# Kernel tuning notes

Measured on AMD Instinct MI355X. Metric: run time of the kernel, lower is better.

## Reference

```python
import jax, jax.numpy as jnp
import numpy as np

SEQ, BATCH, IN_DIM, HID_DIM = 512, 256, 256, 256
NQ = 8
ALPHA = 0.5
MLP_HID = 128


def _linear_init(key, fan_in, fan_out):
    k1, k2 = jax.random.split(key)
    bound = 1.0 / np.sqrt(fan_in)
    W = jax.random.uniform(k1, (fan_in, fan_out), minval=-bound, maxval=bound, dtype=jnp.float32)
    b = jax.random.uniform(k2, (fan_out,), minval=-bound, maxval=bound, dtype=jnp.float32)
    return W, b


def setup_inputs() -> dict:
    key = jax.random.key(0)
    ks = jax.random.split(key, 12)
    cdim = IN_DIM + HID_DIM
    inputs = jax.random.normal(ks[0], (SEQ, BATCH, IN_DIM), dtype=jnp.float32)
    W1, b1 = _linear_init(ks[1], cdim, MLP_HID)
    W2, b2 = _linear_init(ks[2], MLP_HID, NQ * 4)
    Wf, bf = _linear_init(ks[3], cdim, 1)
    Wi, bi = _linear_init(ks[4], cdim, 1)
    Wg, bg = _linear_init(ks[5], cdim, 1)
    Wo, bo = _linear_init(ks[6], cdim, 1)
    rzf = jax.random.normal(ks[7], (NQ,), dtype=jnp.float32)
    rzi = jax.random.normal(ks[8], (NQ,), dtype=jnp.float32)
    rzg = jax.random.normal(ks[9], (NQ,), dtype=jnp.float32)
    rzo = jax.random.normal(ks[10], (NQ,), dtype=jnp.float32)
    return dict(inputs=inputs, W1=W1, b1=b1, W2=W2, b2=b2,
                Wf=Wf, bf=bf, Wi=Wi, bi=bi, Wg=Wg, bg=bg, Wo=Wo, bo=bo,
                rzf=rzf, rzi=rzi, rzg=rzg, rzo=rzo)


def _qgate(theta):
    # Analytic expectations of the RX/RZ/CNOT-chain circuit:
    # <Z_k> = prod_{j<=k} cos(theta_j); rz_params cancel in Z expectations.
    # Returns mean over wires, shape (batch, 1).
    return jnp.mean(jnp.cumprod(jnp.cos(theta), axis=-1), axis=-1, keepdims=True)


def reference(inputs, W1, b1, W2, b2, Wf, bf, Wi, bi, Wg, bg, Wo, bo, rzf, rzi, rzg, rzo):
    batch = inputs.shape[1]
    hx0 = jnp.zeros((batch, HID_DIM), dtype=inputs.dtype)
    cx0 = jnp.zeros((batch, HID_DIM), dtype=inputs.dtype)

    def step(carry, x):
        hx, cx = carry
        combined = jnp.concatenate([x, hx], axis=1)  # (B, in+hid)
        f_c = jax.nn.sigmoid(combined @ Wf + bf)
        i_c = jax.nn.sigmoid(combined @ Wi + bi)
        g_c = jnp.tanh(combined @ Wg + bg)
        o_c = jax.nn.sigmoid(combined @ Wo + bo)
        h1 = jax.nn.relu(combined @ W1 + b1)
        q = h1 @ W2 + b2  # (B, 4*NQ)
        q_f = _qgate(q[:, 0 * NQ:1 * NQ])
        q_i = _qgate(q[:, 1 * NQ:2 * NQ])
        q_g = _qgate(q[:, 2 * NQ:3 * NQ])
        q_o = _qgate(q[:, 3 * NQ:4 * NQ])
        f = (1 - ALPHA) * f_c + ALPHA * jax.nn.sigmoid(q_f)
        i = (1 - ALPHA) * i_c + ALPHA * jax.nn.sigmoid(q_i)
        g = (1 - ALPHA) * g_c + ALPHA * jnp.tanh(q_g)
        o = (1 - ALPHA) * o_c + ALPHA * jax.nn.sigmoid(q_o)
        cx_new = f * cx + i * g
        hx_new = o * jnp.tanh(cx_new)
        return (hx_new, cx_new), hx_new

    (hx, cx), outputs = jax.lax.scan(step, (hx0, cx0), inputs)
    return outputs, (hx, cx)
```

## Files before the change

### kernel.cpp

```cpp
#include <hip/hip_runtime.h>

#define SEQ 512
#define BATCH 256
#define INDIM 256
#define MLP 128
#define M_ROWS (SEQ * BATCH)
#define PRE_STRIDE 136
#define AUX_OFF ((size_t)M_ROWS * PRE_STRIDE)

#define BT_OFF (AUX_OFF + 160)

typedef __attribute__((ext_vector_type(8))) short short8v;
typedef __attribute__((ext_vector_type(4))) float f32x4;

__device__ __forceinline__ unsigned short bf16_rtne(float f) {
  unsigned u = __float_as_uint(f);
  unsigned r = u + 0x7FFFu + ((u >> 16) & 1u);
  return (unsigned short)(r >> 16);
}
__device__ __forceinline__ void cvt2(float f, unsigned short& h,
                                     unsigned short& l) {
  h = bf16_rtne(f);
  l = bf16_rtne(f - __uint_as_float((unsigned)h << 16));
}

__global__ __launch_bounds__(256) void prep_kernel(
    const float* __restrict__ W1,
    const float* __restrict__ Wf, const float* __restrict__ Wi,
    const float* __restrict__ Wg, const float* __restrict__ Wo,
    const float* __restrict__ bf, const float* __restrict__ bi,
    const float* __restrict__ bg, const float* __restrict__ bo,
    const float* __restrict__ b1, float* __restrict__ aux,
    float* __restrict__ btbase) {
  const int tid = threadIdx.x;
  if (tid < 128) {
    float s = 0.f;
    for (int k = 0; k < 256; ++k) s += W1[(size_t)(256 + k) * 128 + tid];
    aux[tid] = s;
  } else if (tid < 132) {
    const int g = tid - 128;
    const float* w = (g == 0) ? Wf : (g == 1) ? Wi : (g == 2) ? Wg : Wo;
    float s = 0.f;
    for (int k = 0; k < 256; ++k) s += w[256 + k];
    aux[128 + g] = s;
  } else if (tid < 136) {
    const int g = tid - 132;
    const float* bp = (g == 0) ? bf : (g == 1) ? bi : (g == 2) ? bg : bo;
    aux[132 + g] = bp[0];
  }

  unsigned short* bth = (unsigned short*)btbase;
  unsigned short* btl = (unsigned short*)(btbase + 18432);
  float* b144 = btbase + 36864;
  for (int tau = tid; tau < 576; tau += 256) {
    const int n = tau >> 2, q = tau & 3;
    const float* wg = (n == 129) ? Wi : (n == 130) ? Wg : (n == 131) ? Wo : Wf;
    for (int k = q * 64; k < q * 64 + 64; ++k) {
      const float v = (n < 128) ? W1[(size_t)k * 128 + n]
                                : ((n < 132) ? wg[k] : 0.f);
      unsigned short h, l;
      cvt2(v, h, l);
      bth[n * 256 + k] = h;
      btl[n * 256 + k] = l;
    }
  }
  if (tid < 144) {
    const float bv = (tid < 128) ? b1[tid]
                   : (tid == 128) ? bf[0] : (tid == 129) ? bi[0]
                   : (tid == 130) ? bg[0] : (tid == 131) ? bo[0] : 0.f;
    b144[tid] = bv;
  }
}

__global__ __attribute__((amdgpu_waves_per_eu(1, 3))) __launch_bounds__(256)
void gemm_kernel(const float* __restrict__ X,
                 const unsigned short* __restrict__ Bth,
                 const unsigned short* __restrict__ Btl,
                 const float* __restrict__ bias144,
                 float* __restrict__ PRE) {
  __shared__ __align__(16) unsigned short Ah[4096];
  __shared__ __align__(16) unsigned short Al[4096];
  __shared__ __align__(16) unsigned short Bh[4608];
  __shared__ __align__(16) unsigned short Bl[4608];

  const int tid = threadIdx.x;
  const size_t rowbase = (size_t)blockIdx.x * 128;
  const int lane = tid & 63, wv = tid >> 6;
  const int l15 = lane & 15, kgl = lane >> 4;
  const int mt0 = wv * 2, mt1 = wv * 2 + 1;

  f32x4 acc0[9], acc1[9];
#pragma unroll
  for (int nt = 0; nt < 9; ++nt) {
    acc0[nt] = (f32x4){0.f, 0.f, 0.f, 0.f};
    acc1[nt] = (f32x4){0.f, 0.f, 0.f, 0.f};
  }

  for (int kc = 0; kc < 256; kc += 32) {
    __syncthreads();
#pragma unroll
    for (int s = 0; s < 2; ++s) {
      const int tau = tid + s * 256;
      const int r = tau >> 2, kg = tau & 3;
      const float4 xa = *(const float4*)&X[(rowbase + r) * 256 + kc + kg * 8];
      const float4 xb =
          *(const float4*)&X[(rowbase + r) * 256 + kc + kg * 8 + 4];
      unsigned short h0, h1, h2, h3, h4, h5, h6, h7;
      unsigned short l0, l1, l2, l3, l4, l5, l6, l7;
      cvt2(xa.x, h0, l0); cvt2(xa.y, h1, l1);
      cvt2(xa.z, h2, l2); cvt2(xa.w, h3, l3);
      cvt2(xb.x, h4, l4); cvt2(xb.y, h5, l5);
      cvt2(xb.z, h6, l6); cvt2(xb.w, h7, l7);
      const short8v hv = {(short)h0, (short)h1, (short)h2, (short)h3,
                          (short)h4, (short)h5, (short)h6, (short)h7};
      const short8v lv = {(short)l0, (short)l1, (short)l2, (short)l3,
                          (short)l4, (short)l5, (short)l6, (short)l7};
      const int dst = (((r >> 4) * 4 + kg) * 16 + (r & 15)) * 8;
      *(short8v*)&Ah[dst] = hv;
      *(short8v*)&Al[dst] = lv;
    }
#pragma unroll
    for (int s = 0; s < 3; ++s) {
      const int tau = tid + s * 256;
      if (tau < 576) {
        const int n = tau >> 2, kg = tau & 3;
        const int src = n * 256 + kc + kg * 8;
        const int dst = (((n >> 4) * 4 + kg) * 16 + (n & 15)) * 8;
        *(short8v*)&Bh[dst] = *(const short8v*)&Bth[src];
        *(short8v*)&Bl[dst] = *(const short8v*)&Btl[src];
      }
    }
    __syncthreads();

    const int ab0 = ((mt0 * 4 + kgl) * 16 + l15) * 8;
    const int ab1 = ((mt1 * 4 + kgl) * 16 + l15) * 8;
    const short8v ah0 = *(const short8v*)&Ah[ab0];
    const short8v al0 = *(const short8v*)&Al[ab0];
    const short8v ah1 = *(const short8v*)&Ah[ab1];
    const short8v al1 = *(const short8v*)&Al[ab1];
#pragma unroll
    for (int nt = 0; nt < 9; ++nt) {
      const int bb = ((nt * 4 + kgl) * 16 + l15) * 8;
      const short8v bh = *(const short8v*)&Bh[bb];
      const short8v bl = *(const short8v*)&Bl[bb];
      acc0[nt] = __builtin_amdgcn_mfma_f32_16x16x32_bf16(ah0, bh, acc0[nt], 0, 0, 0);
      acc0[nt] = __builtin_amdgcn_mfma_f32_16x16x32_bf16(ah0, bl, acc0[nt], 0, 0, 0);
      acc0[nt] = __builtin_amdgcn_mfma_f32_16x16x32_bf16(al0, bh, acc0[nt], 0, 0, 0);
      acc1[nt] = __builtin_amdgcn_mfma_f32_16x16x32_bf16(ah1, bh, acc1[nt], 0, 0, 0);
      acc1[nt] = __builtin_amdgcn_mfma_f32_16x16x32_bf16(ah1, bl, acc1[nt], 0, 0, 0);
      acc1[nt] = __builtin_amdgcn_mfma_f32_16x16x32_bf16(al1, bh, acc1[nt], 0, 0, 0);
    }
  }

#pragma unroll
  for (int nt = 0; nt < 9; ++nt) {
    const int col = nt * 16 + l15;
    if (col < 132) {
      const float bb = bias144[col];
#pragma unroll
      for (int q = 0; q < 4; ++q) {
        PRE[(rowbase + mt0 * 16 + kgl * 4 + q) * PRE_STRIDE + col] =
            acc0[nt][q] + bb;
        PRE[(rowbase + mt1 * 16 + kgl * 4 + q) * PRE_STRIDE + col] =
            acc1[nt][q] + bb;
      }
    }
  }
}

__device__ __forceinline__ float sigmoid_f(float x) {
  return __fdividef(1.0f, 1.0f + __expf(-x));
}
__device__ __forceinline__ float tanh_f(float x) {
  const float e = __expf(-2.0f * x);
  return __fdividef(1.0f - e, 1.0f + e);
}
__device__ __forceinline__ float readlane_f(float v, int lane) {
  return __int_as_float(__builtin_amdgcn_readlane(__float_as_int(v), lane));
}

__global__ __attribute__((amdgpu_waves_per_eu(1, 1))) __launch_bounds__(64)
void rec_kernel(
    const float* __restrict__ PRE, const float* __restrict__ W2,
    const float* __restrict__ b2, const float* __restrict__ aux,
    float* __restrict__ out) {
  __shared__ __align__(16) float h1s[128];

  const int l = threadIdx.x;
  const int b = blockIdx.x;
  const int m = l & 31, half = l >> 5;
  const int g = m >> 3;
  const int g8 = g * 8;

  float w2r[64];
#pragma unroll
  for (int u = 0; u < 64; ++u) w2r[u] = W2[(size_t)(half * 64 + u) * 32 + m];
  const float b2m = b2[m];
  const float2 s1 = *(const float2*)&aux[2 * l];
  const float4 sg = *(const float4*)&aux[128];

  float h = 0.f, c = 0.f;

  const float* pr0 = PRE + (size_t)b * PRE_STRIDE;
  const size_t ts = (size_t)BATCH * PRE_STRIDE;

  float2 p0 = *(const float2*)(pr0 + 0 * ts + 2 * l);
  float4 g0 = *(const float4*)(pr0 + 0 * ts + 128);
  float2 p1 = *(const float2*)(pr0 + 1 * ts + 2 * l);
  float4 g1 = *(const float4*)(pr0 + 1 * ts + 128);

  const float4* h1p = (const float4*)&h1s[half * 64];

  for (int t = 0; t < SEQ; ++t) {
    const float h10 = fmaxf(fmaf(h, s1.x, p0.x), 0.f);
    const float h11 = fmaxf(fmaf(h, s1.y, p0.y), 0.f);

    ((float2*)h1s)[l] = make_float2(h10, h11);
    asm volatile("" ::: "memory");

    const float zf = fmaf(h, sg.x, g0.x);
    const float zi = fmaf(h, sg.y, g0.y);
    const float zg = fmaf(h, sg.z, g0.z);
    const float zo = fmaf(h, sg.w, g0.w);
    const float cf = sigmoid_f(zf);
    const float ci = sigmoid_f(zi);
    const float cg = tanh_f(zg);
    const float co = sigmoid_f(zo);
    p0 = p1; g0 = g1;
    const int tn = (t + 2 < SEQ) ? (t + 2) : (SEQ - 1);
    p1 = *(const float2*)(pr0 + (size_t)tn * ts + 2 * l);
    g1 = *(const float4*)(pr0 + (size_t)tn * ts + 128);

    float q0 = 0.f, q1 = 0.f, q2 = 0.f, q3 = 0.f;
#pragma unroll
    for (int jj = 0; jj < 16; ++jj) {
      const float4 hv = h1p[jj];
      q0 = fmaf(hv.x, w2r[4 * jj + 0], q0);
      q1 = fmaf(hv.y, w2r[4 * jj + 1], q1);
      q2 = fmaf(hv.z, w2r[4 * jj + 2], q2);
      q3 = fmaf(hv.w, w2r[4 * jj + 3], q3);
    }
    const float part = (q0 + q1) + (q2 + q3);

    const float full = part + __shfl_xor(part, 32, 64);
    const float cm = __cosf(full + b2m);
    const int sb = (l & 32) + g8;
    const float e0 = __shfl(cm, sb + 0, 64);
    const float e1 = __shfl(cm, sb + 1, 64);
    const float e2 = __shfl(cm, sb + 2, 64);
    const float e3 = __shfl(cm, sb + 3, 64);
    const float e4 = __shfl(cm, sb + 4, 64);
    const float e5 = __shfl(cm, sb + 5, 64);
    const float e6 = __shfl(cm, sb + 6, 64);
    const float e7 = __shfl(cm, sb + 7, 64);
    float p = e0, s = e0;
    p *= e1; s += p;
    p *= e2; s += p;
    p *= e3; s += p;
    p *= e4; s += p;
    p *= e5; s += p;
    p *= e6; s += p;
    p *= e7; s += p;
    const float qv = s * 0.125f;

    const float qarg = (g == 2) ? (2.0f * qv) : qv;
    const float qs = sigmoid_f(qarg);
    const float av = (g == 2) ? (2.0f * qs - 1.0f) : qs;

    const float aF = readlane_f(av, 0);
    const float aI = readlane_f(av, 8);
    const float aG = readlane_f(av, 16);
    const float aO = readlane_f(av, 24);

    const float f  = 0.5f * (cf + aF);
    const float ii = 0.5f * (ci + aI);
    const float gg = 0.5f * (cg + aG);
    const float oo = 0.5f * (co + aO);

    c = fmaf(f, c, ii * gg);
    h = oo * tanh_f(c);

    float4 hv4o; hv4o.x = h; hv4o.y = h; hv4o.z = h; hv4o.w = h;
    *(float4*)(out + ((size_t)t * BATCH + b) * 256 + 4 * l) = hv4o;
  }

  float4 hq; hq.x = h; hq.y = h; hq.z = h; hq.w = h;
  float4 cq; cq.x = c; cq.y = c; cq.z = c; cq.w = c;
  *(float4*)(out + (size_t)SEQ * BATCH * 256 + (size_t)b * 256 + 4 * l) = hq;
  *(float4*)(out + (size_t)SEQ * BATCH * 256 + (size_t)BATCH * 256 +
             (size_t)b * 256 + 4 * l) = cq;
}

extern "C" void kernel_launch(void* const* d_in, const int* in_sizes, int n_in,
                              void* d_out, int out_size, void* d_ws,
                              size_t ws_size, hipStream_t stream) {
  const float* X  = (const float*)d_in[0];
  const float* W1 = (const float*)d_in[1];
  const float* b1 = (const float*)d_in[2];
  const float* W2 = (const float*)d_in[3];
  const float* b2 = (const float*)d_in[4];
  const float* Wf = (const float*)d_in[5];
  const float* bf = (const float*)d_in[6];
  const float* Wi = (const float*)d_in[7];
  const float* bi = (const float*)d_in[8];
  const float* Wg = (const float*)d_in[9];
  const float* bg = (const float*)d_in[10];
  const float* Wo = (const float*)d_in[11];
  const float* bo = (const float*)d_in[12];

  float* ws  = (float*)d_ws;
  float* PRE = ws;
  float* aux = ws + AUX_OFF;
  float* btbase = ws + BT_OFF;
  const unsigned short* bth = (const unsigned short*)btbase;
  const unsigned short* btl = (const unsigned short*)(btbase + 18432);
  const float* b144 = btbase + 36864;
  float* out = (float*)d_out;

  prep_kernel<<<1, 256, 0, stream>>>(W1, Wf, Wi, Wg, Wo, bf, bi, bg, bo,
                                     b1, aux, btbase);
  gemm_kernel<<<M_ROWS / 128, 256, 0, stream>>>(X, bth, btl, b144, PRE);
  rec_kernel<<<BATCH, 64, 0, stream>>>(PRE, W2, b2, aux, out);
}
```

Measured before the change: 799.8 us.

## Parallelize weight prep across blocks and halve GEMM row tile

The weight prep kernel now runs on 130 blocks. One block computes the aux sums and biases, one converts the gate weights and zeroes the padding rows, and the remaining 128 blocks each transpose and split two rows of W1 into bf16 hi/lo parts. Before, a single block did all of this serially. The GEMM tile drops from 128 to 64 rows per block, giving twice as many blocks with fewer accumulators and less LDS each, and the waves-per-EU hint is raised to allow more occupancy. In exchange, B-tile staging is reused across fewer rows, so B traffic per output row doubles.

Measured after the change: 704.0 us. 1.14x faster.

```diff
diff --git a/kernel.cpp b/kernel.cpp
--- a/kernel.cpp
+++ b/kernel.cpp
@@ -33,75 +33,82 @@
     const float* __restrict__ b1, float* __restrict__ aux,
     float* __restrict__ btbase) {
   const int tid = threadIdx.x;
-  if (tid < 128) {
-    float s = 0.f;
-    for (int k = 0; k < 256; ++k) s += W1[(size_t)(256 + k) * 128 + tid];
-    aux[tid] = s;
-  } else if (tid < 132) {
-    const int g = tid - 128;
-    const float* w = (g == 0) ? Wf : (g == 1) ? Wi : (g == 2) ? Wg : Wo;
-    float s = 0.f;
-    for (int k = 0; k < 256; ++k) s += w[256 + k];
-    aux[128 + g] = s;
-  } else if (tid < 136) {
-    const int g = tid - 132;
-    const float* bp = (g == 0) ? bf : (g == 1) ? bi : (g == 2) ? bg : bo;
-    aux[132 + g] = bp[0];
-  }
-
+  const int blk = blockIdx.x;
   unsigned short* bth = (unsigned short*)btbase;
   unsigned short* btl = (unsigned short*)(btbase + 18432);
   float* b144 = btbase + 36864;
-  for (int tau = tid; tau < 576; tau += 256) {
-    const int n = tau >> 2, q = tau & 3;
-    const float* wg = (n == 129) ? Wi : (n == 130) ? Wg : (n == 131) ? Wo : Wf;
-    for (int k = q * 64; k < q * 64 + 64; ++k) {
-      const float v = (n < 128) ? W1[(size_t)k * 128 + n]
-                                : ((n < 132) ? wg[k] : 0.f);
+
+  if (blk == 0) {
+    if (tid < 128) {
+      float s = 0.f;
+      for (int k = 0; k < 256; ++k) s += W1[(size_t)(256 + k) * 128 + tid];
+      aux[tid] = s;
+    } else if (tid < 132) {
+      const int g = tid - 128;
+      const float* w = (g == 0) ? Wf : (g == 1) ? Wi : (g == 2) ? Wg : Wo;
+      float s = 0.f;
+      for (int k = 0; k < 256; ++k) s += w[256 + k];
+      aux[128 + g] = s;
+    } else if (tid < 136) {
+      const int g = tid - 132;
+      const float* bp = (g == 0) ? bf : (g == 1) ? bi : (g == 2) ? bg : bo;
+      aux[132 + g] = bp[0];
+    }
+    if (tid < 144) {
+      const float bv = (tid < 128) ? b1[tid]
+                     : (tid == 128) ? bf[0] : (tid == 129) ? bi[0]
+                     : (tid == 130) ? bg[0] : (tid == 131) ? bo[0] : 0.f;
+      b144[tid] = bv;
+    }
+  } else if (blk == 1) {
+    for (int idx = tid; idx < 1024; idx += 256) {
+      const int n = 128 + (idx >> 8), k = idx & 255;
+      const float* wg = (n == 128) ? Wf : (n == 129) ? Wi
+                       : (n == 130) ? Wg : Wo;
       unsigned short h, l;
-      cvt2(v, h, l);
+      cvt2(wg[k], h, l);
       bth[n * 256 + k] = h;
       btl[n * 256 + k] = l;
     }
+    for (int idx = tid; idx < 3072; idx += 256) {
+      const int n = 132 + (idx >> 8), k = idx & 255;
+      bth[n * 256 + k] = 0;
+      btl[n * 256 + k] = 0;
+    }
+  } else {
+    const int k = 2 * (blk - 2) + (tid >> 7);
+    const int n = tid & 127;
+    unsigned short h, l;
+    cvt2(W1[(size_t)k * 128 + n], h, l);
+    bth[n * 256 + k] = h;
+    btl[n * 256 + k] = l;
   }
-  if (tid < 144) {
-    const float bv = (tid < 128) ? b1[tid]
-                   : (tid == 128) ? bf[0] : (tid == 129) ? bi[0]
-                   : (tid == 130) ? bg[0] : (tid == 131) ? bo[0] : 0.f;
-    b144[tid] = bv;
-  }
-}
-
-__global__ __attribute__((amdgpu_waves_per_eu(1, 3))) __launch_bounds__(256)
+}
+
+__global__ __attribute__((amdgpu_waves_per_eu(1, 4))) __launch_bounds__(256)
 void gemm_kernel(const float* __restrict__ X,
                  const unsigned short* __restrict__ Bth,
                  const unsigned short* __restrict__ Btl,
                  const float* __restrict__ bias144,
                  float* __restrict__ PRE) {
-  __shared__ __align__(16) unsigned short Ah[4096];
-  __shared__ __align__(16) unsigned short Al[4096];
+  __shared__ __align__(16) unsigned short Ah[2048];
+  __shared__ __align__(16) unsigned short Al[2048];
   __shared__ __align__(16) unsigned short Bh[4608];
   __shared__ __align__(16) unsigned short Bl[4608];
 
   const int tid = threadIdx.x;
-  const size_t rowbase = (size_t)blockIdx.x * 128;
+  const size_t rowbase = (size_t)blockIdx.x * 64;
   const int lane = tid & 63, wv = tid >> 6;
   const int l15 = lane & 15, kgl = lane >> 4;
-  const int mt0 = wv * 2, mt1 = wv * 2 + 1;
-
-  f32x4 acc0[9], acc1[9];
-#pragma unroll
-  for (int nt = 0; nt < 9; ++nt) {
-    acc0[nt] = (f32x4){0.f, 0.f, 0.f, 0.f};
-    acc1[nt] = (f32x4){0.f, 0.f, 0.f, 0.f};
-  }
+
+  f32x4 acc[9];
+#pragma unroll
+  for (int nt = 0; nt < 9; ++nt) acc[nt] = (f32x4){0.f, 0.f, 0.f, 0.f};
 
   for (int kc = 0; kc < 256; kc += 32) {
     __syncthreads();
-#pragma unroll
-    for (int s = 0; s < 2; ++s) {
-      const int tau = tid + s * 256;
-      const int r = tau >> 2, kg = tau & 3;
+    {
+      const int r = tid >> 2, kg = tid & 3;
       const float4 xa = *(const float4*)&X[(rowbase + r) * 256 + kc + kg * 8];
       const float4 xb =
           *(const float4*)&X[(rowbase + r) * 256 + kc + kg * 8 + 4];
@@ -132,23 +139,17 @@
     }
     __syncthreads();
 
-    const int ab0 = ((mt0 * 4 + kgl) * 16 + l15) * 8;
-    const int ab1 = ((mt1 * 4 + kgl) * 16 + l15) * 8;
-    const short8v ah0 = *(const short8v*)&Ah[ab0];
-    const short8v al0 = *(const short8v*)&Al[ab0];
-    const short8v ah1 = *(const short8v*)&Ah[ab1];
-    const short8v al1 = *(const short8v*)&Al[ab1];
+    const int ab = ((wv * 4 + kgl) * 16 + l15) * 8;
+    const short8v ah = *(const short8v*)&Ah[ab];
+    const short8v al = *(const short8v*)&Al[ab];
 #pragma unroll
     for (int nt = 0; nt < 9; ++nt) {
       const int bb = ((nt * 4 + kgl) * 16 + l15) * 8;
       const short8v bh = *(const short8v*)&Bh[bb];
       const short8v bl = *(const short8v*)&Bl[bb];
-      acc0[nt] = __builtin_amdgcn_mfma_f32_16x16x32_bf16(ah0, bh, acc0[nt], 0, 0, 0);
-      acc0[nt] = __builtin_amdgcn_mfma_f32_16x16x32_bf16(ah0, bl, acc0[nt], 0, 0, 0);
-      acc0[nt] = __builtin_amdgcn_mfma_f32_16x16x32_bf16(al0, bh, acc0[nt], 0, 0, 0);
-      acc1[nt] = __builtin_amdgcn_mfma_f32_16x16x32_bf16(ah1, bh, acc1[nt], 0, 0, 0);
-      acc1[nt] = __builtin_amdgcn_mfma_f32_16x16x32_bf16(ah1, bl, acc1[nt], 0, 0, 0);
-      acc1[nt] = __builtin_amdgcn_mfma_f32_16x16x32_bf16(al1, bh, acc1[nt], 0, 0, 0);
+      acc[nt] = __builtin_amdgcn_mfma_f32_16x16x32_bf16(ah, bh, acc[nt], 0, 0, 0);
+      acc[nt] = __builtin_amdgcn_mfma_f32_16x16x32_bf16(ah, bl, acc[nt], 0, 0, 0);
+      acc[nt] = __builtin_amdgcn_mfma_f32_16x16x32_bf16(al, bh, acc[nt], 0, 0, 0);
     }
   }
 
@@ -159,10 +160,8 @@
       const float bb = bias144[col];
 #pragma unroll
       for (int q = 0; q < 4; ++q) {
-        PRE[(rowbase + mt0 * 16 + kgl * 4 + q) * PRE_STRIDE + col] =
-            acc0[nt][q] + bb;
-        PRE[(rowbase + mt1 * 16 + kgl * 4 + q) * PRE_STRIDE + col] =
-            acc1[nt][q] + bb;
+        PRE[(rowbase + wv * 16 + kgl * 4 + q) * PRE_STRIDE + col] =
+            acc[nt][q] + bb;
       }
     }
   }
@@ -317,8 +316,8 @@
   const float* b144 = btbase + 36864;
   float* out = (float*)d_out;
 
-  prep_kernel<<<1, 256, 0, stream>>>(W1, Wf, Wi, Wg, Wo, bf, bi, bg, bo,
-                                     b1, aux, btbase);
-  gemm_kernel<<<M_ROWS / 128, 256, 0, stream>>>(X, bth, btl, b144, PRE);
+  prep_kernel<<<130, 256, 0, stream>>>(W1, Wf, Wi, Wg, Wo, bf, bi, bg, bo,
+                                       b1, aux, btbase);
+  gemm_kernel<<<M_ROWS / 64, 256, 0, stream>>>(X, bth, btl, b144, PRE);
   rec_kernel<<<BATCH, 64, 0, stream>>>(PRE, W2, b2, aux, out);
 }
```
